# Kernel tuning notes

Hardware: AMD Instinct MI355X
Metric: run time of the kernel (lower is better)

The kernel has to match this reference:

```python
import jax, jax.numpy as jnp
import numpy as np

D_MODEL = 768
D_POS = 64
NHEAD = 12
D_FF = 3072
HEAD_DIM = D_MODEL // NHEAD
LN_EPS = 1e-5


def _layer_norm(x, gamma, beta):
    mu = jnp.mean(x, axis=-1, keepdims=True)
    var = jnp.var(x, axis=-1, keepdims=True)
    return (x - mu) * jax.lax.rsqrt(var + LN_EPS) * gamma + beta


def setup_inputs() -> dict:
    key = jax.random.key(0)
    ks = jax.random.split(key, 16)
    L, N = 256, 4
    s = 0.02
    return {
        "src": jax.random.normal(ks[0], (L, N, D_MODEL), jnp.float32),
        "pos": jax.random.normal(ks[1], (N, L, L, D_POS), jnp.float32),
        "q_w": jax.random.normal(ks[2], (D_MODEL, D_MODEL), jnp.float32) * s,
        "q_b": jnp.zeros((D_MODEL,), jnp.float32),
        "k_w": jax.random.normal(ks[3], (D_MODEL, D_MODEL), jnp.float32) * s,
        "k_b": jnp.zeros((D_MODEL,), jnp.float32),
        "v_w": jax.random.normal(ks[4], (D_MODEL, D_MODEL), jnp.float32) * s,
        "v_b": jnp.zeros((D_MODEL,), jnp.float32),
        "p_w": jax.random.normal(ks[5], (D_MODEL, D_POS), jnp.float32) * s,
        "p_b": jnp.zeros((D_MODEL,), jnp.float32),
        "out_w": jax.random.normal(ks[6], (D_MODEL, D_MODEL), jnp.float32) * s,
        "out_b": jnp.zeros((D_MODEL,), jnp.float32),
        "lin1_w": jax.random.normal(ks[7], (D_FF, D_MODEL), jnp.float32) * s,
        "lin1_b": jnp.zeros((D_FF,), jnp.float32),
        "lin2_w": jax.random.normal(ks[8], (D_MODEL, D_FF), jnp.float32) * s,
        "lin2_b": jnp.zeros((D_MODEL,), jnp.float32),
        "n1_g": jnp.ones((D_MODEL,), jnp.float32),
        "n1_b": jnp.zeros((D_MODEL,), jnp.float32),
        "n2_g": jnp.ones((D_MODEL,), jnp.float32),
        "n2_b": jnp.zeros((D_MODEL,), jnp.float32),
    }


def reference(src, pos, q_w, q_b, k_w, k_b, v_w, v_b, p_w, p_b,
              out_w, out_b, lin1_w, lin1_b, lin2_w, lin2_b,
              n1_g, n1_b, n2_g, n2_b):
    L, N, E = src.shape
    H, hd = NHEAD, HEAD_DIM
    scaling = float(hd) ** -0.5

    # projections (F.linear: x @ W.T + b)
    q = (src @ q_w.T + q_b).reshape(L, N, H, hd).transpose(1, 2, 0, 3) * scaling  # (N,H,L,hd)
    k = (src @ k_w.T + k_b).reshape(L, N, H, hd).transpose(1, 2, 0, 3)            # (N,H,L,hd)
    v = (src @ v_w.T + v_b).reshape(L, N, H, hd).transpose(1, 2, 0, 3)            # (N,H,L,hd)
    p = (pos @ p_w.T + p_b).reshape(N, L, L, H, hd)                               # (N,L,L,H,hd)

    # content-content + content-position scores
    scores = jnp.einsum('nhid,nhjd->nhij', q, k) \
           + jnp.einsum('nhid,nijhd->nhij', q, p)                                 # (N,H,L,L)
    attn = jax.nn.softmax(scores, axis=-1)

    ctx = jnp.einsum('nhij,nhjd->nhid', attn, v)          # (N,H,L,hd)
    ctx = ctx.transpose(2, 0, 1, 3).reshape(L, N, E)      # (L,N,E)
    attn_out = ctx @ out_w.T + out_b

    x = _layer_norm(src + attn_out, n1_g, n1_b)
    ff = jax.nn.gelu(x @ lin1_w.T + lin1_b, approximate=False) @ lin2_w.T + lin2_b
    x = _layer_norm(x + ff, n2_g, n2_b)
    return x
```

## Files before the change

### kernel.cpp

```cpp
#include <hip/hip_runtime.h>
#include <hip/hip_bf16.h>
#include <math.h>

typedef __hip_bfloat16 bf16;
typedef unsigned short u16;
typedef __attribute__((ext_vector_type(8))) short bf16x8;
typedef __attribute__((ext_vector_type(4))) float f32x4;

#define L_SEQ 256
#define NB 4
#define EMB 768
#define NH 12
#define DFF 3072
#define HD 64

__device__ __forceinline__ float ldE(const void* p, size_t i, int f32) {
    return f32 ? ((const float*)p)[i] : __bfloat162float(((const bf16*)p)[i]);
}
__device__ __forceinline__ float b2f(u16 v) { return __uint_as_float(((unsigned)v) << 16); }
__device__ __forceinline__ u16 f2b(float v) {
    bf16 h = __float2bfloat16(v);
    return *(u16*)&h;
}

__device__ __forceinline__ void cvt8(u16* dst, const void* s, size_t off, int f32) {
    if (f32) {
        const float* sf = (const float*)s + off;
        #pragma unroll
        for (int t = 0; t < 8; ++t) dst[t] = f2b(sf[t]);
    } else {
        *(uint4*)dst = *(const uint4*)((const u16*)s + off);
    }
}

__device__ __forceinline__ int detect_flag(const void* src, int* lds4) {
    int t = threadIdx.x;
    int wave = t >> 6, lane = t & 63;
    unsigned w = ((const unsigned*)src)[t];
    unsigned e = ((w & 0xFFFFu) >> 7) & 0xFFu;
    unsigned long long m = __ballot(e >= 0xC3u);
    if (lane == 0) lds4[wave] = __popcll(m);
    __syncthreads();
    return (lds4[0] + lds4[1] + lds4[2] + lds4[3]) > 8 ? 1 : 0;
}

__global__ void pack_all(u16* __restrict__ xb, u16* __restrict__ wqkv,
                         u16* __restrict__ owb, u16* __restrict__ l1b,
                         u16* __restrict__ l2b, float* __restrict__ biasf,
                         const void* src, const void* qw, const void* kw, const void* vw,
                         const void* ow, const void* l1w, const void* l2w,
                         const void* qb, const void* kb, const void* vb,
                         const void* ob, const void* b1, const void* b2,
                         int* __restrict__ flagp) {
    __shared__ int lds4[4];
    const int f32 = detect_flag(src, lds4);
    int b = blockIdx.x;
    if (b == 0 && threadIdx.x == 0) *flagp = f32;
    if (b >= 3840) {
        int o = (b - 3840) * 256 + threadIdx.x;
        if (o >= 6912) return;
        float v;
        if (o < 768)       v = ldE(qb, o, f32);
        else if (o < 1536) v = ldE(kb, o - 768, f32);
        else if (o < 2304) v = ldE(vb, o - 1536, f32);
        else if (o < 3072) v = ldE(ob, o - 2304, f32);
        else if (o < 6144) v = ldE(b1, o - 3072, f32);
        else               v = ldE(b2, o - 6144, f32);
        biasf[o] = v;
        return;
    }
    int gid = b * 256 + threadIdx.x;
    u16 tmp[8];
    if (gid < 98304) {
        size_t idx = (size_t)gid * 8;
        cvt8(tmp, src, idx, f32);
        *(uint4*)(xb + idx) = *(uint4*)tmp;
    } else if (gid < 319488) {
        size_t idx = (size_t)(gid - 98304) * 8;
        int r = (int)(idx / EMB);
        const void* s;
        size_t off;
        if (r < EMB)          { s = qw; off = idx; }
        else if (r < 2 * EMB) { s = kw; off = idx - (size_t)EMB * EMB; }
        else                  { s = vw; off = idx - (size_t)2 * EMB * EMB; }
        cvt8(tmp, s, off, f32);
        *(uint4*)(wqkv + idx) = *(uint4*)tmp;
    } else if (gid < 393216) {
        size_t idx = (size_t)(gid - 319488) * 8;
        cvt8(tmp, ow, idx, f32);
        *(uint4*)(owb + idx) = *(uint4*)tmp;
    } else if (gid < 688128) {
        size_t idx = (size_t)(gid - 393216) * 8;
        cvt8(tmp, l1w, idx, f32);
        *(uint4*)(l1b + idx) = *(uint4*)tmp;
    } else {
        size_t idx = (size_t)(gid - 688128) * 8;
        cvt8(tmp, l2w, idx, f32);
        *(uint4*)(l2b + idx) = *(uint4*)tmp;
    }
}

template <int MODE>
__global__ __launch_bounds__(256, 3) void mfma_gemm(
        const u16* __restrict__ A, const u16* __restrict__ W,
        const float* __restrict__ biasf,
        u16* __restrict__ outB0, u16* __restrict__ outB1, u16* __restrict__ outB2,
        float* __restrict__ outF, float* __restrict__ outF2,
        int K, int lda, int ksplit) {
    __shared__ u16 As[64][32];
    __shared__ u16 Ws[64][32];
    int tid = threadIdx.x;
    int wave = tid >> 6, lane = tid & 63;
    int quad = lane >> 4, col = lane & 15;
    int m0 = blockIdx.y * 64, n0 = blockIdx.x * 64;
    int z = blockIdx.z;
    const u16* Ap = A + (size_t)z * ksplit;
    const u16* Wp = W + (size_t)z * ksplit;
    int wm = (wave >> 1) * 32, wn = (wave & 1) * 32;
    f32x4 acc[2][2];
    #pragma unroll
    for (int a = 0; a < 2; ++a)
        #pragma unroll
        for (int b = 0; b < 2; ++b) acc[a][b] = (f32x4){0.f, 0.f, 0.f, 0.f};
    for (int k0 = 0; k0 < K; k0 += 32) {
        {
            int r = tid >> 2, c4 = (tid & 3) * 8;
            const u16* ga = &Ap[(size_t)(m0 + r) * lda + k0 + c4];
            unsigned off = (unsigned)(wave * 64 * 16);
            __builtin_amdgcn_global_load_lds(
                (const __attribute__((address_space(1))) void*)ga,
                (__attribute__((address_space(3))) void*)((char*)&As[0][0] + off),
                16, 0, 0);
        }
        {
            int r = tid >> 2, c4 = (tid & 3) * 8;
            const u16* gw = &Wp[(size_t)(n0 + r) * lda + k0 + c4];
            unsigned off = (unsigned)(wave * 64 * 16);
            __builtin_amdgcn_global_load_lds(
                (const __attribute__((address_space(1))) void*)gw,
                (__attribute__((address_space(3))) void*)((char*)&Ws[0][0] + off),
                16, 0, 0);
        }
        __syncthreads();
        bf16x8 af[2], bfr[2];
        #pragma unroll
        for (int mi = 0; mi < 2; ++mi)
            af[mi] = __builtin_bit_cast(bf16x8, *(const uint4*)&As[wm + mi * 16 + col][quad * 8]);
        #pragma unroll
        for (int ni = 0; ni < 2; ++ni)
            bfr[ni] = __builtin_bit_cast(bf16x8, *(const uint4*)&Ws[wn + ni * 16 + col][quad * 8]);
        #pragma unroll
        for (int mi = 0; mi < 2; ++mi)
            #pragma unroll
            for (int ni = 0; ni < 2; ++ni)
                acc[mi][ni] = __builtin_amdgcn_mfma_f32_16x16x32_bf16(
                    af[mi], bfr[ni], acc[mi][ni], 0, 0, 0);
        __syncthreads();
    }
    #pragma unroll
    for (int mi = 0; mi < 2; ++mi)
        #pragma unroll
        for (int ni = 0; ni < 2; ++ni)
            #pragma unroll
            for (int reg = 0; reg < 4; ++reg) {
                int rr = m0 + wm + mi * 16 + quad * 4 + reg;
                int cc = n0 + wn + ni * 16 + col;
                float v = acc[mi][ni][reg];
                if (MODE == 0) {
                    v += biasf[cc];
                    int i = rr >> 2, n = rr & 3;
                    if (cc < EMB) {
                        int h = cc >> 6, d = cc & 63;
                        outB0[(((size_t)(n * NH + h)) * L_SEQ + i) * HD + d] = f2b(v * 0.125f);
                    } else if (cc < 2 * EMB) {
                        int c2 = cc - EMB;
                        int h = c2 >> 6, d = c2 & 63;
                        outB1[(((size_t)(n * NH + h)) * L_SEQ + i) * HD + d] = f2b(v);
                    } else {
                        outB2[((size_t)n * EMB + (cc - 2 * EMB)) * L_SEQ + i] = f2b(v);
                    }
                } else if (MODE == 2) {
                    v += biasf[cc];
                    v = 0.5f * v * (1.0f + erff(v * 0.70710678118654752f));
                    outB0[(size_t)rr * DFF + cc] = f2b(v);
                } else if (MODE == 4) {
                    float* o = z ? outF2 : outF;
                    o[(size_t)rr * EMB + cc] = v;
                } else {
                    atomicAdd(&outF[(size_t)rr * EMB + cc], v);
                }
            }
}

__global__ __launch_bounds__(256) void qp_kernel(
        const u16* __restrict__ qb, const void* __restrict__ p_w,
        const void* __restrict__ p_b, u16* __restrict__ qp_b,
        float* __restrict__ qpb, const int* __restrict__ flagp) {
    const int f32 = *flagp;
    int w = threadIdx.x >> 6, t = threadIdx.x & 63;
    int blk = blockIdx.x * 4 + w;
    int i = blk & 255;
    int h = (blk >> 8) % NH;
    int n = blk / (256 * NH);
    __shared__ float qs[4][64];
    qs[w][t] = b2f(qb[(((size_t)(n * NH + h)) * L_SEQ + i) * HD + t]);
    __syncthreads();
    float acc = 0.f;
    #pragma unroll 16
    for (int d = 0; d < 64; ++d)
        acc += qs[w][d] * ldE(p_w, (size_t)(h * HD + d) * HD + t, f32);
    qp_b[(((size_t)(n * L_SEQ + i)) * 16 + h) * 64 + t] = f2b(acc);
    float v = qs[w][t] * ldE(p_b, h * HD + t, f32);
    #pragma unroll
    for (int off = 32; off; off >>= 1) v += __shfl_down(v, off);
    if (t == 0) qpb[blk] = v;
}

__global__ __launch_bounds__(64) void s2_mfma(
        const u16* __restrict__ qp_b, const float* __restrict__ qpb,
        const void* __restrict__ pos, float* __restrict__ S,
        const int* __restrict__ flagp) {
    const int f32 = *flagp;
    int wid = blockIdx.x;
    int jh = blockIdx.y;
    int i = wid & 255, n = wid >> 8;
    int lane = threadIdx.x;
    int quad = lane >> 4, col = lane & 15;
    const u16* qprow = qp_b + (((size_t)wid) * 16 + col) * 64;
    bf16x8 a0 = __builtin_bit_cast(bf16x8, *(const uint4*)(qprow + quad * 8));
    bf16x8 a1 = __builtin_bit_cast(bf16x8, *(const uint4*)(qprow + 32 + quad * 8));
    float qpb_r[4];
    #pragma unroll
    for (int reg = 0; reg < 4; ++reg) {
        int h = quad * 4 + reg;
        qpb_r[reg] = (h < NH) ? qpb[((size_t)n * NH + h) * L_SEQ + i] : 0.f;
    }
    #pragma unroll
    for (int tt = 0; tt < 4; ++tt) {
        int t = jh * 4 + tt;
        int j = t * 16 + col;
        size_t pbase = ((size_t)(n * L_SEQ + i) * L_SEQ + j) * HD;
        bf16x8 b0, b1;
        if (f32) {
            const float* pf = (const float*)pos + pbase;
            u16 tmp[16];
            #pragma unroll
            for (int c = 0; c < 8; ++c) tmp[c] = f2b(pf[quad * 8 + c]);
            #pragma unroll
            for (int c = 0; c < 8; ++c) tmp[8 + c] = f2b(pf[32 + quad * 8 + c]);
            b0 = *(bf16x8*)tmp;
            b1 = *(bf16x8*)(tmp + 8);
        } else {
            const u16* pb = (const u16*)pos + pbase;
            b0 = __builtin_bit_cast(bf16x8, *(const uint4*)(pb + quad * 8));
            b1 = __builtin_bit_cast(bf16x8, *(const uint4*)(pb + 32 + quad * 8));
        }
        f32x4 acc = (f32x4){0.f, 0.f, 0.f, 0.f};
        acc = __builtin_amdgcn_mfma_f32_16x16x32_bf16(a0, b0, acc, 0, 0, 0);
        acc = __builtin_amdgcn_mfma_f32_16x16x32_bf16(a1, b1, acc, 0, 0, 0);
        if (quad < 3) {
            #pragma unroll
            for (int reg = 0; reg < 4; ++reg) {
                int h = quad * 4 + reg;
                S[(((size_t)n * NH + h) * L_SEQ + i) * L_SEQ + j] = acc[reg] + qpb_r[reg];
            }
        }
    }
}

__global__ __launch_bounds__(256) void attn3_kernel(
        const u16* __restrict__ qb, const u16* __restrict__ kb,
        const u16* __restrict__ vt, const float* __restrict__ S,
        u16* __restrict__ ctxb) {
    __shared__ u16 p_lds[16][268];
    __shared__ float lds_m[4][16];
    __shared__ float lds_s[4][16];
    int b = blockIdx.x;
    int n = b / (NH * 16), rem = b % (NH * 16), h = rem >> 4, it = rem & 15;
    int wave = threadIdx.x >> 6, lane = threadIdx.x & 63;
    int quad = lane >> 4, col = lane & 15;
    int i0 = it * 16;

    const u16* qh = qb + ((size_t)(n * NH + h)) * L_SEQ * HD;
    const u16* kh = kb + ((size_t)(n * NH + h)) * L_SEQ * HD;

    const u16* qrow = qh + (size_t)(i0 + col) * HD;
    bf16x8 a0 = __builtin_bit_cast(bf16x8, *(const uint4*)(qrow + quad * 8));
    bf16x8 a1 = __builtin_bit_cast(bf16x8, *(const uint4*)(qrow + 32 + quad * 8));

    f32x4 sc[4];
    #pragma unroll
    for (int tt = 0; tt < 4; ++tt) {
        int t = wave * 4 + tt;
        const u16* krow = kh + (size_t)(t * 16 + col) * HD;
        bf16x8 b0 = __builtin_bit_cast(bf16x8, *(const uint4*)(krow + quad * 8));
        bf16x8 b1 = __builtin_bit_cast(bf16x8, *(const uint4*)(krow + 32 + quad * 8));
        f32x4 acc = (f32x4){0.f, 0.f, 0.f, 0.f};
        acc = __builtin_amdgcn_mfma_f32_16x16x32_bf16(a0, b0, acc, 0, 0, 0);
        acc = __builtin_amdgcn_mfma_f32_16x16x32_bf16(a1, b1, acc, 0, 0, 0);
        sc[tt] = acc;
    }

    #pragma unroll
    for (int reg = 0; reg < 4; ++reg) {
        const float* Srow = S + (((size_t)n * NH + h) * L_SEQ + i0 + quad * 4 + reg) * L_SEQ + col;
        float m = -1e30f;
        #pragma unroll
        for (int tt = 0; tt < 4; ++tt) {
            float v = sc[tt][reg] + Srow[(wave * 4 + tt) * 16];
            sc[tt][reg] = v;
            m = fmaxf(m, v);
        }
        #pragma unroll
        for (int off = 1; off < 16; off <<= 1) m = fmaxf(m, __shfl_xor(m, off));
        if (col == 0) lds_m[wave][quad * 4 + reg] = m;
    }
    __syncthreads();
    float gm[4];
    #pragma unroll
    for (int reg = 0; reg < 4; ++reg) {
        int row = quad * 4 + reg;
        gm[reg] = fmaxf(fmaxf(lds_m[0][row], lds_m[1][row]),
                        fmaxf(lds_m[2][row], lds_m[3][row]));
    }
    #pragma unroll
    for (int reg = 0; reg < 4; ++reg) {
        float sum = 0.f;
        #pragma unroll
        for (int tt = 0; tt < 4; ++tt) {
            float e = __expf(sc[tt][reg] - gm[reg]);
            sc[tt][reg] = e;
            sum += e;
        }
        #pragma unroll
        for (int off = 1; off < 16; off <<= 1) sum += __shfl_xor(sum, off);
        if (col == 0) lds_s[wave][quad * 4 + reg] = sum;
    }
    __syncthreads();
    #pragma unroll
    for (int reg = 0; reg < 4; ++reg) {
        int row = quad * 4 + reg;
        float gs = lds_s[0][row] + lds_s[1][row] + lds_s[2][row] + lds_s[3][row];
        float inv = 1.0f / gs;
        #pragma unroll
        for (int tt = 0; tt < 4; ++tt)
            p_lds[row][(wave * 4 + tt) * 16 + col] = f2b(sc[tt][reg] * inv);
    }
    __syncthreads();

    bf16x8 ap[8];
    #pragma unroll
    for (int kt = 0; kt < 8; ++kt)
        ap[kt] = __builtin_bit_cast(bf16x8, *(const uint4*)&p_lds[col][kt * 32 + quad * 8]);
    {
        const u16* vrow = vt + ((size_t)n * EMB + h * HD + wave * 16 + col) * L_SEQ;
        f32x4 acc = (f32x4){0.f, 0.f, 0.f, 0.f};
        #pragma unroll
        for (int kt = 0; kt < 8; ++kt) {
            bf16x8 bp = __builtin_bit_cast(bf16x8, *(const uint4*)(vrow + kt * 32 + quad * 8));
            acc = __builtin_amdgcn_mfma_f32_16x16x32_bf16(ap[kt], bp, acc, 0, 0, 0);
        }
        #pragma unroll
        for (int reg = 0; reg < 4; ++reg) {
            int ii = i0 + quad * 4 + reg;
            ctxb[((size_t)ii * NB + n) * EMB + h * HD + wave * 16 + col] = f2b(acc[reg]);
        }
    }
}

__device__ __forceinline__ float blk_sum(float v, volatile float* ws, int wave, int lane) {
    #pragma unroll
    for (int off = 32; off; off >>= 1) v += __shfl_xor(v, off);
    if (lane == 0) ws[wave] = v;
    __syncthreads();
    float s = ws[0] + ws[1] + ws[2] + ws[3];
    __syncthreads();
    return s;
}

__global__ void ln1_kernel(const float* __restrict__ p0, const float* __restrict__ p1,
                           const void* __restrict__ src, const float* __restrict__ biasf,
                           const void* __restrict__ g, const void* __restrict__ b,
                           u16* __restrict__ x1b, float* __restrict__ y2,
                           const int* __restrict__ flagp) {
    const int f32 = *flagp;
    int r = blockIdx.x;
    int t = threadIdx.x;
    int wave = t >> 6, lane = t & 63;
    __shared__ float ws[4];
    float x[3];
    #pragma unroll
    for (int p = 0; p < 3; ++p) {
        int e = t + p * 256;
        size_t oi = (size_t)r * EMB + e;
        x[p] = p0[oi] + p1[oi] + ldE(src, oi, f32) + biasf[2304 + e];
    }
    float mean = blk_sum(x[0] + x[1] + x[2], ws, wave, lane) * (1.0f / EMB);
    float d0 = x[0] - mean, d1 = x[1] - mean, d2 = x[2] - mean;
    float var = blk_sum(d0 * d0 + d1 * d1 + d2 * d2, ws, wave, lane) * (1.0f / EMB);
    float rstd = rsqrtf(var + 1e-5f);
    float vs[3] = {d0, d1, d2};
    #pragma unroll
    for (int p = 0; p < 3; ++p) {
        int e = t + p * 256;
        float v = vs[p] * rstd * ldE(g, e, f32) + ldE(b, e, f32);
        size_t oi = (size_t)r * EMB + e;
        x1b[oi] = f2b(v);
        y2[oi] = v + biasf[6144 + e];
    }
}

__global__ void ln2_kernel(const float* __restrict__ X, const void* __restrict__ g,
                           const void* __restrict__ b, void* __restrict__ outAny,
                           const int* __restrict__ flagp) {
    const int f32 = *flagp;
    int r = blockIdx.x;
    int t = threadIdx.x;
    int wave = t >> 6, lane = t & 63;
    __shared__ float ws[4];
    float x0 = X[(size_t)r * EMB + t];
    float x1 = X[(size_t)r * EMB + t + 256];
    float x2 = X[(size_t)r * EMB + t + 512];
    float mean = blk_sum(x0 + x1 + x2, ws, wave, lane) * (1.0f / EMB);
    float d0 = x0 - mean, d1 = x1 - mean, d2 = x2 - mean;
    float var = blk_sum(d0 * d0 + d1 * d1 + d2 * d2, ws, wave, lane) * (1.0f / EMB);
    float rstd = rsqrtf(var + 1e-5f);
    float vs[3] = {d0, d1, d2};
    #pragma unroll
    for (int p = 0; p < 3; ++p) {
        int e = t + p * 256;
        float v = vs[p] * rstd * ldE(g, e, f32) + ldE(b, e, f32);
        size_t oi = (size_t)r * EMB + e;
        if (f32) ((float*)outAny)[oi] = v;
        else     ((bf16*)outAny)[oi] = __float2bfloat16(v);
    }
}

extern "C" void kernel_launch(void* const* d_in, const int* in_sizes, int n_in,
                              void* d_out, int out_size, void* d_ws, size_t ws_size,
                              hipStream_t stream) {
    const void* src    = d_in[0];
    const void* pos    = d_in[1];
    const void* q_w    = d_in[2];
    const void* q_b    = d_in[3];
    const void* k_w    = d_in[4];
    const void* k_b    = d_in[5];
    const void* v_w    = d_in[6];
    const void* v_b    = d_in[7];
    const void* p_w    = d_in[8];
    const void* p_b    = d_in[9];
    const void* out_w  = d_in[10];
    const void* out_b  = d_in[11];
    const void* lin1_w = d_in[12];
    const void* lin1_b = d_in[13];
    const void* lin2_w = d_in[14];
    const void* lin2_b = d_in[15];
    const void* n1_g   = d_in[16];
    const void* n1_b   = d_in[17];
    const void* n2_g   = d_in[18];
    const void* n2_b   = d_in[19];

    float* f = (float*)d_ws;
    int*   flagp = (int*)f;
    float* biasf = f + 16;
    u16*   xb    = (u16*)(f + 6928);
    u16*   wqkv  = (u16*)(f + 400144);
    u16*   owb   = (u16*)(f + 1284880);
    u16*   l1b   = (u16*)(f + 1579792);
    u16*   l2b   = (u16*)(f + 2759440);
    u16*   qbp   = (u16*)(f + 3939088);
    u16*   kbp   = (u16*)(f + 4332304);
    u16*   vtb   = (u16*)(f + 4725520);
    u16*   qp_b  = (u16*)(f + 5118736);
    float* qpb   = f + 5643024;
    float* S     = f + 5655312;
    u16*   ctxb  = (u16*)(f + 8801040);
    u16*   ffb   = (u16*)S;
    float* y2    = S + 1572864;
    float* pOut1 = S + 2359296;
    float* pOut0 = f + 400144;
    u16*   x1b   = vtb;

    pack_all<<<3867, 256, 0, stream>>>(xb, wqkv, owb, l1b, l2b, biasf,
                                       src, q_w, k_w, v_w, out_w, lin1_w, lin2_w,
                                       q_b, k_b, v_b, out_b, lin1_b, lin2_b, flagp);

    mfma_gemm<0><<<dim3(36, 16), 256, 0, stream>>>(
        xb, wqkv, biasf, qbp, kbp, vtb, nullptr, nullptr, EMB, EMB, 0);

    qp_kernel<<<NB * NH * L_SEQ / 4, 256, 0, stream>>>(qbp, p_w, p_b, qp_b, qpb, flagp);
    s2_mfma<<<dim3(NB * L_SEQ, 4), 64, 0, stream>>>(qp_b, qpb, pos, S, flagp);

    attn3_kernel<<<NB * NH * 16, 256, 0, stream>>>(qbp, kbp, vtb, S, ctxb);

    mfma_gemm<4><<<dim3(12, 16, 2), 256, 0, stream>>>(
        ctxb, owb, nullptr, nullptr, nullptr, nullptr, pOut0, pOut1, 384, EMB, 384);

    ln1_kernel<<<1024, 256, 0, stream>>>(pOut0, pOut1, src, biasf, n1_g, n1_b,
                                         x1b, y2, flagp);

    mfma_gemm<2><<<dim3(48, 16), 256, 0, stream>>>(
        x1b, l1b, biasf + 3072, ffb, nullptr, nullptr, nullptr, nullptr, EMB, EMB, 0);

    mfma_gemm<5><<<dim3(12, 16, 4), 256, 0, stream>>>(
        ffb, l2b, nullptr, nullptr, nullptr, nullptr, y2, nullptr, 768, DFF, 768);

    ln2_kernel<<<1024, 256, 0, stream>>>(y2, n2_g, n2_b, d_out, flagp);
}
```

Before: 263.9 us.

## Fuse q·p_w projection into position-score MFMA kernel via LDS

Merges the qp_kernel and s2_mfma kernels into one kernel, one block per (n,i) row. Each block's four waves compute all heads' q·p_w projections and bias terms into shared memory, then each wave runs the MFMA over a quarter of the j positions. This drops one launch and the global round trip for the qp intermediates. Each block now repeats the projection work once for its row, reading p_w again instead of reusing a precomputed buffer. Separately, the GEMM launch bound is raised from 3 to 4 blocks per CU to increase occupancy, at the risk of register spills.

```diff
diff --git a/kernel.cpp b/kernel.cpp
--- a/kernel.cpp
+++ b/kernel.cpp
@@ -101,7 +101,7 @@
 }
 
 template <int MODE>
-__global__ __launch_bounds__(256, 3) void mfma_gemm(
+__global__ __launch_bounds__(256, 4) void mfma_gemm(
         const u16* __restrict__ A, const u16* __restrict__ W,
         const float* __restrict__ biasf,
         u16* __restrict__ outB0, u16* __restrict__ outB1, u16* __restrict__ outB2,
@@ -192,52 +192,51 @@
             }
 }
 
-__global__ __launch_bounds__(256) void qp_kernel(
+__global__ __launch_bounds__(256) void s2qp_kernel(
         const u16* __restrict__ qb, const void* __restrict__ p_w,
-        const void* __restrict__ p_b, u16* __restrict__ qp_b,
-        float* __restrict__ qpb, const int* __restrict__ flagp) {
+        const void* __restrict__ p_b, const void* __restrict__ pos,
+        float* __restrict__ S, const int* __restrict__ flagp) {
     const int f32 = *flagp;
-    int w = threadIdx.x >> 6, t = threadIdx.x & 63;
-    int blk = blockIdx.x * 4 + w;
-    int i = blk & 255;
-    int h = (blk >> 8) % NH;
-    int n = blk / (256 * NH);
-    __shared__ float qs[4][64];
-    qs[w][t] = b2f(qb[(((size_t)(n * NH + h)) * L_SEQ + i) * HD + t]);
-    __syncthreads();
-    float acc = 0.f;
-    #pragma unroll 16
-    for (int d = 0; d < 64; ++d)
-        acc += qs[w][d] * ldE(p_w, (size_t)(h * HD + d) * HD + t, f32);
-    qp_b[(((size_t)(n * L_SEQ + i)) * 16 + h) * 64 + t] = f2b(acc);
-    float v = qs[w][t] * ldE(p_b, h * HD + t, f32);
-    #pragma unroll
-    for (int off = 32; off; off >>= 1) v += __shfl_down(v, off);
-    if (t == 0) qpb[blk] = v;
-}
-
-__global__ __launch_bounds__(64) void s2_mfma(
-        const u16* __restrict__ qp_b, const float* __restrict__ qpb,
-        const void* __restrict__ pos, float* __restrict__ S,
-        const int* __restrict__ flagp) {
-    const int f32 = *flagp;
+    __shared__ float qs_lds[16][64];
+    __shared__ u16 qp_lds[16][72];
+    __shared__ float qpb_lds[16];
     int wid = blockIdx.x;
-    int jh = blockIdx.y;
     int i = wid & 255, n = wid >> 8;
-    int lane = threadIdx.x;
+    int wave = threadIdx.x >> 6, lane = threadIdx.x & 63;
+
+    #pragma unroll
+    for (int r = 0; r < 4; ++r) {
+        int h = wave * 4 + r;
+        qs_lds[h][lane] = (h < NH)
+            ? b2f(qb[(((size_t)(n * NH + h)) * L_SEQ + i) * HD + lane]) : 0.f;
+    }
+    __syncthreads();
+    #pragma unroll
+    for (int r = 0; r < 4; ++r) {
+        int h = wave * 4 + r;
+        float acc = 0.f;
+        if (h < NH) {
+            #pragma unroll 16
+            for (int d = 0; d < 64; ++d)
+                acc += qs_lds[h][d] * ldE(p_w, (size_t)(h * HD + d) * HD + lane, f32);
+        }
+        qp_lds[h][lane] = f2b(acc);
+        float v = (h < NH) ? qs_lds[h][lane] * ldE(p_b, h * HD + lane, f32) : 0.f;
+        #pragma unroll
+        for (int off = 32; off; off >>= 1) v += __shfl_down(v, off);
+        if (lane == 0) qpb_lds[h] = v;
+    }
+    __syncthreads();
+
     int quad = lane >> 4, col = lane & 15;
-    const u16* qprow = qp_b + (((size_t)wid) * 16 + col) * 64;
-    bf16x8 a0 = __builtin_bit_cast(bf16x8, *(const uint4*)(qprow + quad * 8));
-    bf16x8 a1 = __builtin_bit_cast(bf16x8, *(const uint4*)(qprow + 32 + quad * 8));
+    bf16x8 a0 = __builtin_bit_cast(bf16x8, *(const uint4*)&qp_lds[col][quad * 8]);
+    bf16x8 a1 = __builtin_bit_cast(bf16x8, *(const uint4*)&qp_lds[col][32 + quad * 8]);
     float qpb_r[4];
     #pragma unroll
-    for (int reg = 0; reg < 4; ++reg) {
-        int h = quad * 4 + reg;
-        qpb_r[reg] = (h < NH) ? qpb[((size_t)n * NH + h) * L_SEQ + i] : 0.f;
-    }
+    for (int reg = 0; reg < 4; ++reg) qpb_r[reg] = qpb_lds[quad * 4 + reg];
     #pragma unroll
     for (int tt = 0; tt < 4; ++tt) {
-        int t = jh * 4 + tt;
+        int t = wave * 4 + tt;
         int j = t * 16 + col;
         size_t pbase = ((size_t)(n * L_SEQ + i) * L_SEQ + j) * HD;
         bf16x8 b0, b1;
@@ -471,8 +470,6 @@
     u16*   qbp   = (u16*)(f + 3939088);
     u16*   kbp   = (u16*)(f + 4332304);
     u16*   vtb   = (u16*)(f + 4725520);
-    u16*   qp_b  = (u16*)(f + 5118736);
-    float* qpb   = f + 5643024;
     float* S     = f + 5655312;
     u16*   ctxb  = (u16*)(f + 8801040);
     u16*   ffb   = (u16*)S;
@@ -488,8 +485,7 @@
     mfma_gemm<0><<<dim3(36, 16), 256, 0, stream>>>(
         xb, wqkv, biasf, qbp, kbp, vtb, nullptr, nullptr, EMB, EMB, 0);
 
-    qp_kernel<<<NB * NH * L_SEQ / 4, 256, 0, stream>>>(qbp, p_w, p_b, qp_b, qpb, flagp);
-    s2_mfma<<<dim3(NB * L_SEQ, 4), 64, 0, stream>>>(qp_b, qpb, pos, S, flagp);
+    s2qp_kernel<<<NB * L_SEQ, 256, 0, stream>>>(qbp, p_w, p_b, pos, S, flagp);
 
     attn3_kernel<<<NB * NH * 16, 256, 0, stream>>>(qbp, kbp, vtb, S, ctxb);
 
```

After: 270.0 us. 2.3% more time.
